# Performance work log

Hardware: AMD Instinct MI355X
Metric: run time of the kernel (lower is better)

## Reference

```python
import jax, jax.numpy as jnp
import numpy as np

DIM = 128
NUM_HEADS = 4
WIN = 16  # effective window: window_size(8) * sqrt(dim_t=4)
N = WIN * WIN
B_ = 512
NW = 64


def _relative_position_index(wh, ww):
    coords = np.stack(np.meshgrid(np.arange(wh), np.arange(ww), indexing='ij'))  # (2,wh,ww)
    cf = coords.reshape(2, -1)
    rel = cf[:, :, None] - cf[:, None, :]  # (2,N,N)
    rel = rel.transpose(1, 2, 0).copy()
    rel[:, :, 0] += wh - 1
    rel[:, :, 1] += ww - 1
    rel[:, :, 0] *= 2 * ww - 1
    return rel.sum(-1).astype(np.int32)  # (N,N)


def setup_inputs() -> dict:
    key = jax.random.key(0)
    ks = jax.random.split(key, 7)
    inputs = jax.random.normal(ks[0], (B_, N, DIM), dtype=jnp.float32)
    mask = jax.random.normal(ks[1], (NW, N, N), dtype=jnp.float32)
    qkv_w = jax.random.normal(ks[2], (3 * DIM, DIM), dtype=jnp.float32) * 0.02
    qkv_b = jnp.zeros((3 * DIM,), dtype=jnp.float32)
    proj_w = jax.random.normal(ks[3], (DIM, DIM), dtype=jnp.float32) * 0.02
    proj_b = jnp.zeros((DIM,), dtype=jnp.float32)
    table_sz = (2 * WIN - 1) * (2 * WIN - 1)  # 961
    bias_table = jax.random.normal(ks[4], (table_sz, NUM_HEADS), dtype=jnp.float32) * 0.02
    rel_idx = jnp.asarray(_relative_position_index(WIN, WIN))  # (N,N) int32
    return {"inputs": inputs, "mask": mask, "qkv_w": qkv_w, "qkv_b": qkv_b,
            "proj_w": proj_w, "proj_b": proj_b, "bias_table": bias_table,
            "rel_idx": rel_idx}


def reference(inputs, mask, qkv_w, qkv_b, proj_w, proj_b, bias_table, rel_idx):
    B, Nn, C = inputs.shape
    H = bias_table.shape[1]
    Dh = C // H
    scale = Dh ** -0.5
    qkv = (inputs @ qkv_w.T + qkv_b).reshape(B, Nn, 3, H, Dh)
    qkv = jnp.transpose(qkv, (2, 0, 3, 1, 4))  # (3,B,H,N,Dh)
    q, k, v = qkv[0] * scale, qkv[1], qkv[2]
    attn = jnp.einsum('bhnd,bhmd->bhnm', q, k)  # (B,H,N,N)
    rpb = jnp.transpose(bias_table[rel_idx], (2, 0, 1))  # (H,N,N)
    attn = attn + rpb[None]
    nW = mask.shape[0]
    attn = attn.reshape(B // nW, nW, H, Nn, Nn) + mask[None, :, None]
    attn = jax.nn.softmax(attn.reshape(B, H, Nn, Nn), axis=-1)
    out = jnp.einsum('bhnm,bhmd->bhnd', attn, v)
    out = jnp.transpose(out, (0, 2, 1, 3)).reshape(B, Nn, C)
    return out @ proj_w.T + proj_b
```

## Files before the change

kernel.cpp:

```cpp
#include <hip/hip_runtime.h>

typedef __bf16 bf16;
typedef __bf16 bf16x8 __attribute__((ext_vector_type(8)));
typedef __bf16 bf16x4 __attribute__((ext_vector_type(4)));
typedef float f32x4 __attribute__((ext_vector_type(4)));

static __device__ __forceinline__ f32x4 mfma16(bf16x8 a, bf16x8 b, f32x4 c) {
  return __builtin_amdgcn_mfma_f32_16x16x32_bf16(a, b, c, 0, 0, 0);
}

static __device__ __forceinline__ bf16x8 ld_bf8(const float* __restrict__ p) {
  f32x4 a = *(const f32x4*)p;
  f32x4 b = *(const f32x4*)(p + 4);
  bf16x8 r;
  r[0] = (bf16)a[0]; r[1] = (bf16)a[1]; r[2] = (bf16)a[2]; r[3] = (bf16)a[3];
  r[4] = (bf16)b[0]; r[5] = (bf16)b[1]; r[6] = (bf16)b[2]; r[7] = (bf16)b[3];
  return r;
}

__global__ void k0w(const float* __restrict__ qw, const float* __restrict__ pw,
                    bf16* __restrict__ wb, bf16* __restrict__ pwb) {
  int t = blockIdx.x * 256 + threadIdx.x;
  if (t < 12288) {
    f32x4 v = *(const f32x4*)(qw + (size_t)t * 4);
    bf16x4 o;
#pragma unroll
    for (int r = 0; r < 4; ++r) o[r] = (bf16)v[r];
    *(bf16x4*)(wb + (size_t)t * 4) = o;
  } else {
    int u = t - 12288;
    f32x4 v = *(const f32x4*)(pw + (size_t)u * 4);
    bf16x4 o;
#pragma unroll
    for (int r = 0; r < 4; ++r) o[r] = (bf16)v[r];
    *(bf16x4*)(pwb + (size_t)u * 4) = o;
  }
}

__global__ void __launch_bounds__(256, 4)
k1f(const float* __restrict__ x, const bf16* __restrict__ wb,
    const float* __restrict__ qb, bf16* __restrict__ q_s, bf16* __restrict__ k_s,
    bf16* __restrict__ vt, const float* __restrict__ mask,
    const float* __restrict__ bt, const int* __restrict__ ri,
    bf16* __restrict__ mb, bf16* __restrict__ rb) {
  const int bid = blockIdx.x;
  const int tid = threadIdx.x;
  if (bid >= 2048) {
    if (bid < 3072) {
      const int mid = bid - 2048;
#pragma unroll
      for (int it = 0; it < 4; ++it) {
        const size_t t = (size_t)mid * 1024 + it * 256 + tid;
        f32x4 m4 = *(const f32x4*)(mask + t * 4);
        bf16x4 o;
#pragma unroll
        for (int r = 0; r < 4; ++r) o[r] = (bf16)m4[r];
        *(bf16x4*)(mb + t * 4) = o;
      }
    } else {
      const int t = (bid - 3072) * 256 + tid;
      const int idx = ri[t];
      f32x4 v = *(const f32x4*)(bt + idx * 4);
#pragma unroll
      for (int h = 0; h < 4; ++h) rb[h * 65536 + t] = (bf16)v[h];
    }
    return;
  }

  const int b = bid & 511, qt = bid >> 9;
  const int wv = tid >> 6, ln = tid & 15, qd = (tid >> 4) & 3;
  const int row0 = qt * 64 + (wv >> 1) * 32;
  const int cg = wv & 1;

  bf16x8 xf[2][4];
#pragma unroll
  for (int nt = 0; nt < 2; ++nt)
#pragma unroll
    for (int ks = 0; ks < 4; ++ks)
      xf[nt][ks] = ld_bf8(x + (size_t)(b * 256 + row0 + nt * 16 + ln) * 128 +
                          ks * 32 + qd * 8);

#pragma unroll
  for (int ch = 0; ch < 2; ++ch) {
    f32x4 acc[4][2];
#pragma unroll
    for (int mt = 0; mt < 4; ++mt)
#pragma unroll
      for (int nt = 0; nt < 2; ++nt) acc[mt][nt] = (f32x4){0.f, 0.f, 0.f, 0.f};
#pragma unroll
    for (int mt = 0; mt < 4; ++mt)
#pragma unroll
      for (int ks = 0; ks < 4; ++ks) {
        bf16x8 wf = *(const bf16x8*)(wb + (size_t)(ch * 128 + cg * 64 + mt * 16 + ln) *
                                              128 + ks * 32 + qd * 8);
#pragma unroll
        for (int nt = 0; nt < 2; ++nt) acc[mt][nt] = mfma16(wf, xf[nt][ks], acc[mt][nt]);
      }
    bf16* dst = ch ? k_s : q_s;
    const float scl = ch ? 1.0f : 0.17677669529663689f;
#pragma unroll
    for (int mt = 0; mt < 4; ++mt) {
      const int c0 = cg * 64 + mt * 16 + qd * 4;
      f32x4 b4 = *(const f32x4*)(qb + ch * 128 + c0);
      const int hh = c0 >> 5, d0 = c0 & 31;
#pragma unroll
      for (int nt = 0; nt < 2; ++nt) {
        const int nr = row0 + nt * 16 + ln;
        bf16x4 o;
#pragma unroll
        for (int r = 0; r < 4; ++r) o[r] = (bf16)((acc[mt][nt][r] + b4[r]) * scl);
        *(bf16x4*)(dst + (size_t)((b * 4 + hh) * 256 + nr) * 32 + d0) = o;
      }
    }
  }

  f32x4 av[2][4];
#pragma unroll
  for (int nt = 0; nt < 2; ++nt)
#pragma unroll
    for (int mt = 0; mt < 4; ++mt) av[nt][mt] = (f32x4){0.f, 0.f, 0.f, 0.f};
#pragma unroll
  for (int ks = 0; ks < 4; ++ks)
#pragma unroll
    for (int mt = 0; mt < 4; ++mt) {
      bf16x8 wf = *(const bf16x8*)(wb + (size_t)(256 + cg * 64 + mt * 16 + ln) * 128 +
                                   ks * 32 + qd * 8);
#pragma unroll
      for (int nt = 0; nt < 2; ++nt) av[nt][mt] = mfma16(xf[nt][ks], wf, av[nt][mt]);
    }
#pragma unroll
  for (int nt = 0; nt < 2; ++nt)
#pragma unroll
    for (int mt = 0; mt < 4; ++mt) {
      const int c = cg * 64 + mt * 16 + ln;
      const float bb = qb[256 + c];
      const int hh = c >> 5, dd = c & 31;
      const int n0 = row0 + nt * 16 + qd * 4;
      bf16x4 o;
#pragma unroll
      for (int r = 0; r < 4; ++r) o[r] = (bf16)(av[nt][mt][r] + bb);
      *(bf16x4*)(vt + (size_t)((b * 4 + hh) * 32 + dd) * 256 + n0) = o;
    }
}

__global__ void __launch_bounds__(256, 2)
k2_attn(bf16* __restrict__ q_s, const bf16* __restrict__ k_s,
        const bf16* __restrict__ vt, const bf16* __restrict__ mb,
        const bf16* __restrict__ rb) {
  __shared__ bf16 ksm[256 * 32];
  __shared__ bf16 vsm[32 * 256];
  __shared__ bf16 psm[4 * 16 * 256];
  const int tid = threadIdx.x, wv = tid >> 6;
  const int ln = tid & 15, qd = (tid >> 4) & 3;
  const int w = blockIdx.x & 63, h = (blockIdx.x >> 6) & 3, rh = blockIdx.x >> 8;

  bf16x4 cmb[2][16];
#pragma unroll
  for (int si = 0; si < 2; ++si) {
    const int n = (rh * 8 + wv * 2 + si) * 16 + ln;
#pragma unroll
    for (int mt = 0; mt < 16; ++mt) {
      bf16x4 m4 = *(const bf16x4*)(mb + (size_t)(w * 256 + n) * 256 + mt * 16 + qd * 4);
      bf16x4 r4 = *(const bf16x4*)(rb + (size_t)h * 65536 + n * 256 + mt * 16 + qd * 4);
      bf16x4 cv;
#pragma unroll
      for (int r = 0; r < 4; ++r) cv[r] = (bf16)((float)m4[r] + (float)r4[r]);
      cmb[si][mt] = cv;
    }
  }

  for (int ib = 0; ib < 8; ++ib) {
    const int b = w + ib * 64;
    const bf16* kp = k_s + (size_t)(b * 4 + h) * 8192;
    const bf16* vp = vt + (size_t)(b * 4 + h) * 8192;
    __syncthreads();
#pragma unroll
    for (int i = 0; i < 4; ++i) {
      const int ci = i * 256 + tid;
      {
        const int r_ = ci >> 2, cb = ci & 3;
        *(bf16x8*)(ksm + r_ * 32 + ((cb ^ (r_ & 3)) * 8)) =
            *(const bf16x8*)(kp + r_ * 32 + cb * 8);
      }
      {
        const int r_ = ci >> 5, cb = ci & 31;
        *(bf16x8*)(vsm + r_ * 256 + ((cb ^ (r_ & 7)) * 8)) =
            *(const bf16x8*)(vp + r_ * 256 + cb * 8);
      }
    }
    __syncthreads();

#pragma unroll
    for (int si = 0; si < 2; ++si) {
      const int s = rh * 8 + wv * 2 + si;
      bf16x8 qf = *(const bf16x8*)(q_s + (size_t)(b * 4 + h) * 8192 +
                                   (s * 16 + ln) * 32 + qd * 8);
      f32x4 acc[16];
#pragma unroll
      for (int mt = 0; mt < 16; ++mt) acc[mt] = (f32x4){0.f, 0.f, 0.f, 0.f};
#pragma unroll
      for (int mt = 0; mt < 16; ++mt) {
        const int m = mt * 16 + ln;
        bf16x8 af = *(const bf16x8*)(ksm + m * 32 + ((qd ^ (m & 3)) * 8));
        acc[mt] = mfma16(af, qf, acc[mt]);
      }
      float sum = 0.f;
      bf16* pb = psm + wv * 4096 + ln * 256;
#pragma unroll
      for (int mt = 0; mt < 16; ++mt) {
        bf16x4 pv;
#pragma unroll
        for (int r = 0; r < 4; ++r) {
          float p = __expf(acc[mt][r] + (float)cmb[si][mt][r]);
          sum += p;
          pv[r] = (bf16)p;
        }
        *(bf16x4*)(pb + (((mt * 2 + (qd >> 1)) ^ (ln & 7)) * 8) + (qd & 1) * 4) = pv;
      }
      sum += __shfl_xor(sum, 16);
      sum += __shfl_xor(sum, 32);
      const float linv = 1.0f / sum;

      f32x4 accO[2];
      accO[0] = (f32x4){0.f, 0.f, 0.f, 0.f};
      accO[1] = (f32x4){0.f, 0.f, 0.f, 0.f};
#pragma unroll
      for (int kt = 0; kt < 8; ++kt) {
        bf16x8 pf = *(const bf16x8*)(pb + (((kt * 4 + qd) ^ (ln & 7)) * 8));
#pragma unroll
        for (int ct = 0; ct < 2; ++ct) {
          const int d = ct * 16 + ln;
          bf16x8 vf = *(const bf16x8*)(vsm + d * 256 + (((kt * 4 + qd) ^ (d & 7)) * 8));
          accO[ct] = mfma16(pf, vf, accO[ct]);
        }
      }
#pragma unroll
      for (int r = 0; r < 4; ++r) {
        const float lb = __shfl(linv, qd * 4 + r);
        const size_t obase =
            (size_t)(b * 4 + h) * 8192 + (size_t)(s * 16 + qd * 4 + r) * 32;
#pragma unroll
        for (int ct = 0; ct < 2; ++ct)
          q_s[obase + ct * 16 + ln] = (bf16)(accO[ct][r] * lb);
      }
    }
  }
}

__global__ void __launch_bounds__(256, 4)
k3_proj(const bf16* __restrict__ xb, const bf16* __restrict__ pwb,
        const float* __restrict__ pbias, float* __restrict__ out) {
  const int bid = blockIdx.x;
  const int b = bid & 511, qt = bid >> 9;
  const int tid = threadIdx.x;
  const int wv = tid >> 6, ln = tid & 15, qd = (tid >> 4) & 3;
  const int cg = wv & 1;
  const int row0 = qt * 64 + (wv >> 1) * 32;

  bf16x8 xf[2][4];
#pragma unroll
  for (int nt = 0; nt < 2; ++nt) {
    const int n = row0 + nt * 16 + ln;
#pragma unroll
    for (int ks = 0; ks < 4; ++ks)
      xf[nt][ks] = *(const bf16x8*)(xb + ((size_t)(b * 4 + ks) * 256 + n) * 32 + qd * 8);
  }

  f32x4 acc[4][2];
#pragma unroll
  for (int mt = 0; mt < 4; ++mt)
#pragma unroll
    for (int nt = 0; nt < 2; ++nt) acc[mt][nt] = (f32x4){0.f, 0.f, 0.f, 0.f};
#pragma unroll
  for (int mt = 0; mt < 4; ++mt)
#pragma unroll
    for (int ks = 0; ks < 4; ++ks) {
      bf16x8 wf = *(const bf16x8*)(pwb + (size_t)(cg * 64 + mt * 16 + ln) * 128 +
                                   ks * 32 + qd * 8);
#pragma unroll
      for (int nt = 0; nt < 2; ++nt) acc[mt][nt] = mfma16(wf, xf[nt][ks], acc[mt][nt]);
    }
#pragma unroll
  for (int mt = 0; mt < 4; ++mt) {
    const int c0 = cg * 64 + mt * 16 + qd * 4;
    f32x4 b4 = *(const f32x4*)(pbias + c0);
#pragma unroll
    for (int nt = 0; nt < 2; ++nt) {
      f32x4 o;
#pragma unroll
      for (int r = 0; r < 4; ++r) o[r] = acc[mt][nt][r] + b4[r];
      *(f32x4*)(out + (size_t)(b * 256 + row0 + nt * 16 + ln) * 128 + c0) = o;
    }
  }
}

extern "C" void kernel_launch(void* const* d_in, const int* in_sizes, int n_in,
                              void* d_out, int out_size, void* d_ws, size_t ws_size,
                              hipStream_t stream) {
  const float* x = (const float*)d_in[0];
  const float* mask = (const float*)d_in[1];
  const float* qkv_w = (const float*)d_in[2];
  const float* qkv_b = (const float*)d_in[3];
  const float* proj_w = (const float*)d_in[4];
  const float* proj_b = (const float*)d_in[5];
  const float* bias_table = (const float*)d_in[6];
  const int* rel_idx = (const int*)d_in[7];

  char* ws = (char*)d_ws;
  bf16* q_s = (bf16*)ws;
  bf16* k_s = (bf16*)(ws + 33554432);
  bf16* vt = (bf16*)(ws + 2ll * 33554432);
  bf16* wb = (bf16*)(ws + 3ll * 33554432);
  bf16* pwb = (bf16*)(ws + 3ll * 33554432 + 98304);
  bf16* mb = (bf16*)d_out;
  bf16* rb = (bf16*)((char*)d_out + 16777216);

  k0w<<<dim3(64), dim3(256), 0, stream>>>(qkv_w, proj_w, wb, pwb);
  k1f<<<dim3(3328), dim3(256), 0, stream>>>(x, wb, qkv_b, q_s, k_s, vt, mask,
                                            bias_table, rel_idx, mb, rb);
  k2_attn<<<dim3(512), dim3(256), 0, stream>>>(q_s, k_s, vt, mb, rb);
  k3_proj<<<dim3(2048), dim3(256), 0, stream>>>(q_s, pwb, proj_b, (float*)d_out);
}
```

Before: 303.6 us.

## Fuse QKV projection, window attention and output projection into one kernel

Replaces the separate QKV, attention and projection kernels with one kernel per batch window of 512 threads. Each block computes Q/K/V per head straight into shared memory, runs attention, and accumulates the output projection in registers before writing the final fp32 output. This removes the global round-trips of Q, K, V and the attention output. It also drops the bf16 mask pre-conversion and reads the fp32 mask directly each time. The cost is heavier per-block work, more register pressure, and repeated mask reads across heads.

```diff
diff --git a/kernel.cpp b/kernel.cpp
--- a/kernel.cpp
+++ b/kernel.cpp
@@ -18,280 +18,233 @@
   return r;
 }
 
-__global__ void k0w(const float* __restrict__ qw, const float* __restrict__ pw,
-                    bf16* __restrict__ wb, bf16* __restrict__ pwb) {
-  int t = blockIdx.x * 256 + threadIdx.x;
-  if (t < 12288) {
-    f32x4 v = *(const f32x4*)(qw + (size_t)t * 4);
-    bf16x4 o;
-#pragma unroll
-    for (int r = 0; r < 4; ++r) o[r] = (bf16)v[r];
-    *(bf16x4*)(wb + (size_t)t * 4) = o;
+__global__ void k0_prep(const float* __restrict__ qw, const float* __restrict__ pw,
+                        const float* __restrict__ bt, const int* __restrict__ ri,
+                        bf16* __restrict__ wb, bf16* __restrict__ pwb,
+                        bf16* __restrict__ rb) {
+  const int t = blockIdx.x * 256 + threadIdx.x;
+  if (blockIdx.x < 64) {
+    if (t < 12288) {
+      f32x4 v = *(const f32x4*)(qw + (size_t)t * 4);
+      bf16x4 o;
+#pragma unroll
+      for (int r = 0; r < 4; ++r) o[r] = (bf16)v[r];
+      *(bf16x4*)(wb + (size_t)t * 4) = o;
+    } else {
+      const int u = t - 12288;
+      f32x4 v = *(const f32x4*)(pw + (size_t)u * 4);
+      bf16x4 o;
+#pragma unroll
+      for (int r = 0; r < 4; ++r) o[r] = (bf16)v[r];
+      *(bf16x4*)(pwb + (size_t)u * 4) = o;
+    }
   } else {
-    int u = t - 12288;
-    f32x4 v = *(const f32x4*)(pw + (size_t)u * 4);
-    bf16x4 o;
-#pragma unroll
-    for (int r = 0; r < 4; ++r) o[r] = (bf16)v[r];
-    *(bf16x4*)(pwb + (size_t)u * 4) = o;
+    const int t2 = t - 16384;
+    const int idx = ri[t2];
+    f32x4 v = *(const f32x4*)(bt + idx * 4);
+#pragma unroll
+    for (int h = 0; h < 4; ++h) rb[h * 65536 + t2] = (bf16)v[h];
   }
 }
 
-__global__ void __launch_bounds__(256, 4)
-k1f(const float* __restrict__ x, const bf16* __restrict__ wb,
-    const float* __restrict__ qb, bf16* __restrict__ q_s, bf16* __restrict__ k_s,
-    bf16* __restrict__ vt, const float* __restrict__ mask,
-    const float* __restrict__ bt, const int* __restrict__ ri,
-    bf16* __restrict__ mb, bf16* __restrict__ rb) {
-  const int bid = blockIdx.x;
-  const int tid = threadIdx.x;
-  if (bid >= 2048) {
-    if (bid < 3072) {
-      const int mid = bid - 2048;
-#pragma unroll
-      for (int it = 0; it < 4; ++it) {
-        const size_t t = (size_t)mid * 1024 + it * 256 + tid;
-        f32x4 m4 = *(const f32x4*)(mask + t * 4);
-        bf16x4 o;
-#pragma unroll
-        for (int r = 0; r < 4; ++r) o[r] = (bf16)m4[r];
-        *(bf16x4*)(mb + t * 4) = o;
-      }
-    } else {
-      const int t = (bid - 3072) * 256 + tid;
-      const int idx = ri[t];
-      f32x4 v = *(const f32x4*)(bt + idx * 4);
-#pragma unroll
-      for (int h = 0; h < 4; ++h) rb[h * 65536 + t] = (bf16)v[h];
-    }
-    return;
-  }
-
-  const int b = bid & 511, qt = bid >> 9;
-  const int wv = tid >> 6, ln = tid & 15, qd = (tid >> 4) & 3;
-  const int row0 = qt * 64 + (wv >> 1) * 32;
-  const int cg = wv & 1;
-
-  bf16x8 xf[2][4];
-#pragma unroll
-  for (int nt = 0; nt < 2; ++nt)
-#pragma unroll
-    for (int ks = 0; ks < 4; ++ks)
-      xf[nt][ks] = ld_bf8(x + (size_t)(b * 256 + row0 + nt * 16 + ln) * 128 +
-                          ks * 32 + qd * 8);
-
-#pragma unroll
-  for (int ch = 0; ch < 2; ++ch) {
-    f32x4 acc[4][2];
-#pragma unroll
-    for (int mt = 0; mt < 4; ++mt)
-#pragma unroll
-      for (int nt = 0; nt < 2; ++nt) acc[mt][nt] = (f32x4){0.f, 0.f, 0.f, 0.f};
-#pragma unroll
-    for (int mt = 0; mt < 4; ++mt)
-#pragma unroll
-      for (int ks = 0; ks < 4; ++ks) {
-        bf16x8 wf = *(const bf16x8*)(wb + (size_t)(ch * 128 + cg * 64 + mt * 16 + ln) *
-                                              128 + ks * 32 + qd * 8);
-#pragma unroll
-        for (int nt = 0; nt < 2; ++nt) acc[mt][nt] = mfma16(wf, xf[nt][ks], acc[mt][nt]);
-      }
-    bf16* dst = ch ? k_s : q_s;
-    const float scl = ch ? 1.0f : 0.17677669529663689f;
-#pragma unroll
-    for (int mt = 0; mt < 4; ++mt) {
-      const int c0 = cg * 64 + mt * 16 + qd * 4;
-      f32x4 b4 = *(const f32x4*)(qb + ch * 128 + c0);
-      const int hh = c0 >> 5, d0 = c0 & 31;
-#pragma unroll
-      for (int nt = 0; nt < 2; ++nt) {
-        const int nr = row0 + nt * 16 + ln;
-        bf16x4 o;
-#pragma unroll
-        for (int r = 0; r < 4; ++r) o[r] = (bf16)((acc[mt][nt][r] + b4[r]) * scl);
-        *(bf16x4*)(dst + (size_t)((b * 4 + hh) * 256 + nr) * 32 + d0) = o;
-      }
-    }
-  }
-
-  f32x4 av[2][4];
-#pragma unroll
-  for (int nt = 0; nt < 2; ++nt)
-#pragma unroll
-    for (int mt = 0; mt < 4; ++mt) av[nt][mt] = (f32x4){0.f, 0.f, 0.f, 0.f};
-#pragma unroll
-  for (int ks = 0; ks < 4; ++ks)
-#pragma unroll
-    for (int mt = 0; mt < 4; ++mt) {
-      bf16x8 wf = *(const bf16x8*)(wb + (size_t)(256 + cg * 64 + mt * 16 + ln) * 128 +
-                                   ks * 32 + qd * 8);
-#pragma unroll
-      for (int nt = 0; nt < 2; ++nt) av[nt][mt] = mfma16(xf[nt][ks], wf, av[nt][mt]);
-    }
-#pragma unroll
-  for (int nt = 0; nt < 2; ++nt)
-#pragma unroll
-    for (int mt = 0; mt < 4; ++mt) {
-      const int c = cg * 64 + mt * 16 + ln;
-      const float bb = qb[256 + c];
-      const int hh = c >> 5, dd = c & 31;
-      const int n0 = row0 + nt * 16 + qd * 4;
-      bf16x4 o;
-#pragma unroll
-      for (int r = 0; r < 4; ++r) o[r] = (bf16)(av[nt][mt][r] + bb);
-      *(bf16x4*)(vt + (size_t)((b * 4 + hh) * 32 + dd) * 256 + n0) = o;
-    }
-}
-
-__global__ void __launch_bounds__(256, 2)
-k2_attn(bf16* __restrict__ q_s, const bf16* __restrict__ k_s,
-        const bf16* __restrict__ vt, const bf16* __restrict__ mb,
-        const bf16* __restrict__ rb) {
+__global__ void __launch_bounds__(512, 2)
+k_main(const float* __restrict__ x, const bf16* __restrict__ wb,
+       const float* __restrict__ qb, const bf16* __restrict__ pwb,
+       const float* __restrict__ pbias, const float* __restrict__ mask,
+       const bf16* __restrict__ rb, float* __restrict__ out) {
   __shared__ bf16 ksm[256 * 32];
   __shared__ bf16 vsm[32 * 256];
-  __shared__ bf16 psm[4 * 16 * 256];
+  __shared__ bf16 psm[8 * 2048];
   const int tid = threadIdx.x, wv = tid >> 6;
   const int ln = tid & 15, qd = (tid >> 4) & 3;
-  const int w = blockIdx.x & 63, h = (blockIdx.x >> 6) & 3, rh = blockIdx.x >> 8;
-
-  bf16x4 cmb[2][16];
-#pragma unroll
-  for (int si = 0; si < 2; ++si) {
-    const int n = (rh * 8 + wv * 2 + si) * 16 + ln;
-#pragma unroll
-    for (int mt = 0; mt < 16; ++mt) {
-      bf16x4 m4 = *(const bf16x4*)(mb + (size_t)(w * 256 + n) * 256 + mt * 16 + qd * 4);
-      bf16x4 r4 = *(const bf16x4*)(rb + (size_t)h * 65536 + n * 256 + mt * 16 + qd * 4);
-      bf16x4 cv;
-#pragma unroll
-      for (int r = 0; r < 4; ++r) cv[r] = (bf16)((float)m4[r] + (float)r4[r]);
-      cmb[si][mt] = cv;
-    }
-  }
-
-  for (int ib = 0; ib < 8; ++ib) {
-    const int b = w + ib * 64;
-    const bf16* kp = k_s + (size_t)(b * 4 + h) * 8192;
-    const bf16* vp = vt + (size_t)(b * 4 + h) * 8192;
+  const int b = blockIdx.x, w = b & 63;
+  bf16* pw_ = psm + wv * 2048;
+
+  bf16x8 xf[2][4];
+#pragma unroll
+  for (int nt = 0; nt < 2; ++nt)
+#pragma unroll
+    for (int ks = 0; ks < 4; ++ks)
+      xf[nt][ks] = ld_bf8(x + (size_t)(b * 256 + wv * 32 + nt * 16 + ln) * 128 +
+                          ks * 32 + qd * 8);
+
+  f32x4 acc_out[2][8];
+#pragma unroll
+  for (int si = 0; si < 2; ++si)
+#pragma unroll
+    for (int ct2 = 0; ct2 < 8; ++ct2) acc_out[si][ct2] = (f32x4){0.f, 0.f, 0.f, 0.f};
+
+  for (int h = 0; h < 4; ++h) {
+    {
+      f32x4 aq[2][2];
+#pragma unroll
+      for (int ct = 0; ct < 2; ++ct)
+#pragma unroll
+        for (int nt = 0; nt < 2; ++nt) aq[ct][nt] = (f32x4){0.f, 0.f, 0.f, 0.f};
+#pragma unroll
+      for (int ct = 0; ct < 2; ++ct)
+#pragma unroll
+        for (int ks = 0; ks < 4; ++ks) {
+          bf16x8 wf = *(const bf16x8*)(wb + (size_t)(h * 32 + ct * 16 + ln) * 128 +
+                                       ks * 32 + qd * 8);
+#pragma unroll
+          for (int nt = 0; nt < 2; ++nt) aq[ct][nt] = mfma16(wf, xf[nt][ks], aq[ct][nt]);
+        }
+#pragma unroll
+      for (int ct = 0; ct < 2; ++ct) {
+        const int c0 = ct * 16 + qd * 4;
+        f32x4 b4 = *(const f32x4*)(qb + h * 32 + c0);
+#pragma unroll
+        for (int nt = 0; nt < 2; ++nt) {
+          bf16x4 o;
+#pragma unroll
+          for (int r = 0; r < 4; ++r)
+            o[r] = (bf16)((aq[ct][nt][r] + b4[r]) * 0.17677669529663689f);
+          *(bf16x4*)(pw_ + (nt * 16 + ln) * 32 + c0) = o;
+        }
+      }
+    }
+    bf16x8 qf0 = *(const bf16x8*)(pw_ + (0 * 16 + ln) * 32 + qd * 8);
+    bf16x8 qf1 = *(const bf16x8*)(pw_ + (1 * 16 + ln) * 32 + qd * 8);
+
     __syncthreads();
-#pragma unroll
-    for (int i = 0; i < 4; ++i) {
-      const int ci = i * 256 + tid;
-      {
-        const int r_ = ci >> 2, cb = ci & 3;
-        *(bf16x8*)(ksm + r_ * 32 + ((cb ^ (r_ & 3)) * 8)) =
-            *(const bf16x8*)(kp + r_ * 32 + cb * 8);
-      }
-      {
-        const int r_ = ci >> 5, cb = ci & 31;
-        *(bf16x8*)(vsm + r_ * 256 + ((cb ^ (r_ & 7)) * 8)) =
-            *(const bf16x8*)(vp + r_ * 256 + cb * 8);
-      }
+
+    {
+      f32x4 ak[2][2];
+#pragma unroll
+      for (int ct = 0; ct < 2; ++ct)
+#pragma unroll
+        for (int nt = 0; nt < 2; ++nt) ak[ct][nt] = (f32x4){0.f, 0.f, 0.f, 0.f};
+#pragma unroll
+      for (int ct = 0; ct < 2; ++ct)
+#pragma unroll
+        for (int ks = 0; ks < 4; ++ks) {
+          bf16x8 wf = *(const bf16x8*)(wb + (size_t)(128 + h * 32 + ct * 16 + ln) * 128 +
+                                       ks * 32 + qd * 8);
+#pragma unroll
+          for (int nt = 0; nt < 2; ++nt) ak[ct][nt] = mfma16(wf, xf[nt][ks], ak[ct][nt]);
+        }
+#pragma unroll
+      for (int ct = 0; ct < 2; ++ct) {
+        const int c0 = ct * 16 + qd * 4;
+        f32x4 b4 = *(const f32x4*)(qb + 128 + h * 32 + c0);
+        const int slot = ct * 2 + (qd >> 1), off = (qd & 1) * 4;
+#pragma unroll
+        for (int nt = 0; nt < 2; ++nt) {
+          const int grow = wv * 32 + nt * 16 + ln;
+          bf16x4 o;
+#pragma unroll
+          for (int r = 0; r < 4; ++r) o[r] = (bf16)(ak[ct][nt][r] + b4[r]);
+          *(bf16x4*)(ksm + grow * 32 + ((slot ^ (grow & 3)) * 8) + off) = o;
+        }
+      }
+      f32x4 av[2][2];
+#pragma unroll
+      for (int nt = 0; nt < 2; ++nt)
+#pragma unroll
+        for (int ct = 0; ct < 2; ++ct) av[nt][ct] = (f32x4){0.f, 0.f, 0.f, 0.f};
+#pragma unroll
+      for (int ks = 0; ks < 4; ++ks)
+#pragma unroll
+        for (int ct = 0; ct < 2; ++ct) {
+          bf16x8 wf = *(const bf16x8*)(wb + (size_t)(256 + h * 32 + ct * 16 + ln) * 128 +
+                                       ks * 32 + qd * 8);
+#pragma unroll
+          for (int nt = 0; nt < 2; ++nt) av[nt][ct] = mfma16(xf[nt][ks], wf, av[nt][ct]);
+        }
+#pragma unroll
+      for (int nt = 0; nt < 2; ++nt)
+#pragma unroll
+        for (int ct = 0; ct < 2; ++ct) {
+          const int c = ct * 16 + ln;
+          const float bb = qb[256 + h * 32 + c];
+          const int n0 = wv * 32 + nt * 16 + qd * 4;
+          const int slot = n0 >> 3, off = (qd & 1) * 4;
+          bf16x4 o;
+#pragma unroll
+          for (int r = 0; r < 4; ++r) o[r] = (bf16)(av[nt][ct][r] + bb);
+          *(bf16x4*)(vsm + c * 256 + ((slot ^ (c & 7)) * 8) + off) = o;
+        }
     }
     __syncthreads();
 
 #pragma unroll
     for (int si = 0; si < 2; ++si) {
-      const int s = rh * 8 + wv * 2 + si;
-      bf16x8 qf = *(const bf16x8*)(q_s + (size_t)(b * 4 + h) * 8192 +
-                                   (s * 16 + ln) * 32 + qd * 8);
-      f32x4 acc[16];
-#pragma unroll
-      for (int mt = 0; mt < 16; ++mt) acc[mt] = (f32x4){0.f, 0.f, 0.f, 0.f};
-#pragma unroll
-      for (int mt = 0; mt < 16; ++mt) {
-        const int m = mt * 16 + ln;
-        bf16x8 af = *(const bf16x8*)(ksm + m * 32 + ((qd ^ (m & 3)) * 8));
-        acc[mt] = mfma16(af, qf, acc[mt]);
-      }
+      const bf16x8 qf = si ? qf1 : qf0;
+      const int n = wv * 32 + si * 16 + ln;
       float sum = 0.f;
-      bf16* pb = psm + wv * 4096 + ln * 256;
-#pragma unroll
-      for (int mt = 0; mt < 16; ++mt) {
-        bf16x4 pv;
-#pragma unroll
-        for (int r = 0; r < 4; ++r) {
-          float p = __expf(acc[mt][r] + (float)cmb[si][mt][r]);
-          sum += p;
-          pv[r] = (bf16)p;
-        }
-        *(bf16x4*)(pb + (((mt * 2 + (qd >> 1)) ^ (ln & 7)) * 8) + (qd & 1) * 4) = pv;
+      f32x4 accO[2];
+      accO[0] = (f32x4){0.f, 0.f, 0.f, 0.f};
+      accO[1] = (f32x4){0.f, 0.f, 0.f, 0.f};
+#pragma unroll
+      for (int hf = 0; hf < 2; ++hf) {
+        f32x4 acc[8];
+#pragma unroll
+        for (int mt = 0; mt < 8; ++mt) acc[mt] = (f32x4){0.f, 0.f, 0.f, 0.f};
+#pragma unroll
+        for (int mt = 0; mt < 8; ++mt) {
+          const int m = hf * 128 + mt * 16 + ln;
+          bf16x8 af = *(const bf16x8*)(ksm + m * 32 + ((qd ^ (m & 3)) * 8));
+          acc[mt] = mfma16(af, qf, acc[mt]);
+        }
+#pragma unroll
+        for (int mt = 0; mt < 8; ++mt) {
+          const int mcol = hf * 128 + mt * 16 + qd * 4;
+          f32x4 m4 = *(const f32x4*)(mask + ((size_t)w * 256 + n) * 256 + mcol);
+          bf16x4 r4 = *(const bf16x4*)(rb + (size_t)h * 65536 + n * 256 + mcol);
+          bf16x4 pv;
+#pragma unroll
+          for (int r = 0; r < 4; ++r) {
+            float p = __expf(acc[mt][r] + m4[r] + (float)r4[r]);
+            sum += p;
+            pv[r] = (bf16)p;
+          }
+          *(bf16x4*)(pw_ + ln * 128 + (((mt * 2 + (qd >> 1)) ^ (ln & 7)) * 8) +
+                     (qd & 1) * 4) = pv;
+        }
+#pragma unroll
+        for (int ktl = 0; ktl < 4; ++ktl) {
+          const int kt = hf * 4 + ktl;
+          bf16x8 pf = *(const bf16x8*)(pw_ + ln * 128 + (((ktl * 4 + qd) ^ (ln & 7)) * 8));
+#pragma unroll
+          for (int ct = 0; ct < 2; ++ct) {
+            const int d = ct * 16 + ln;
+            bf16x8 vf = *(const bf16x8*)(vsm + d * 256 + (((kt * 4 + qd) ^ (d & 7)) * 8));
+            accO[ct] = mfma16(pf, vf, accO[ct]);
+          }
+        }
       }
       sum += __shfl_xor(sum, 16);
       sum += __shfl_xor(sum, 32);
       const float linv = 1.0f / sum;
-
-      f32x4 accO[2];
-      accO[0] = (f32x4){0.f, 0.f, 0.f, 0.f};
-      accO[1] = (f32x4){0.f, 0.f, 0.f, 0.f};
-#pragma unroll
-      for (int kt = 0; kt < 8; ++kt) {
-        bf16x8 pf = *(const bf16x8*)(pb + (((kt * 4 + qd) ^ (ln & 7)) * 8));
-#pragma unroll
-        for (int ct = 0; ct < 2; ++ct) {
-          const int d = ct * 16 + ln;
-          bf16x8 vf = *(const bf16x8*)(vsm + d * 256 + (((kt * 4 + qd) ^ (d & 7)) * 8));
-          accO[ct] = mfma16(pf, vf, accO[ct]);
-        }
-      }
 #pragma unroll
       for (int r = 0; r < 4; ++r) {
         const float lb = __shfl(linv, qd * 4 + r);
-        const size_t obase =
-            (size_t)(b * 4 + h) * 8192 + (size_t)(s * 16 + qd * 4 + r) * 32;
 #pragma unroll
         for (int ct = 0; ct < 2; ++ct)
-          q_s[obase + ct * 16 + ln] = (bf16)(accO[ct][r] * lb);
+          pw_[(qd * 4 + r) * 40 + ct * 16 + ln] = (bf16)(accO[ct][r] * lb);
+      }
+      bf16x8 aof = *(const bf16x8*)(pw_ + ln * 40 + qd * 8);
+#pragma unroll
+      for (int ct2 = 0; ct2 < 8; ++ct2) {
+        bf16x8 wpf = *(const bf16x8*)(pwb + (size_t)(ct2 * 16 + ln) * 128 + h * 32 +
+                                      qd * 8);
+        acc_out[si][ct2] = mfma16(aof, wpf, acc_out[si][ct2]);
       }
     }
   }
-}
-
-__global__ void __launch_bounds__(256, 4)
-k3_proj(const bf16* __restrict__ xb, const bf16* __restrict__ pwb,
-        const float* __restrict__ pbias, float* __restrict__ out) {
-  const int bid = blockIdx.x;
-  const int b = bid & 511, qt = bid >> 9;
-  const int tid = threadIdx.x;
-  const int wv = tid >> 6, ln = tid & 15, qd = (tid >> 4) & 3;
-  const int cg = wv & 1;
-  const int row0 = qt * 64 + (wv >> 1) * 32;
-
-  bf16x8 xf[2][4];
-#pragma unroll
-  for (int nt = 0; nt < 2; ++nt) {
-    const int n = row0 + nt * 16 + ln;
-#pragma unroll
-    for (int ks = 0; ks < 4; ++ks)
-      xf[nt][ks] = *(const bf16x8*)(xb + ((size_t)(b * 4 + ks) * 256 + n) * 32 + qd * 8);
-  }
-
-  f32x4 acc[4][2];
-#pragma unroll
-  for (int mt = 0; mt < 4; ++mt)
-#pragma unroll
-    for (int nt = 0; nt < 2; ++nt) acc[mt][nt] = (f32x4){0.f, 0.f, 0.f, 0.f};
-#pragma unroll
-  for (int mt = 0; mt < 4; ++mt)
-#pragma unroll
-    for (int ks = 0; ks < 4; ++ks) {
-      bf16x8 wf = *(const bf16x8*)(pwb + (size_t)(cg * 64 + mt * 16 + ln) * 128 +
-                                   ks * 32 + qd * 8);
-#pragma unroll
-      for (int nt = 0; nt < 2; ++nt) acc[mt][nt] = mfma16(wf, xf[nt][ks], acc[mt][nt]);
-    }
-#pragma unroll
-  for (int mt = 0; mt < 4; ++mt) {
-    const int c0 = cg * 64 + mt * 16 + qd * 4;
-    f32x4 b4 = *(const f32x4*)(pbias + c0);
-#pragma unroll
-    for (int nt = 0; nt < 2; ++nt) {
-      f32x4 o;
-#pragma unroll
-      for (int r = 0; r < 4; ++r) o[r] = acc[mt][nt][r] + b4[r];
-      *(f32x4*)(out + (size_t)(b * 256 + row0 + nt * 16 + ln) * 128 + c0) = o;
-    }
-  }
+
+#pragma unroll
+  for (int si = 0; si < 2; ++si)
+#pragma unroll
+    for (int ct2 = 0; ct2 < 8; ++ct2) {
+      const int col = ct2 * 16 + ln;
+      const float bb = pbias[col];
+#pragma unroll
+      for (int r = 0; r < 4; ++r)
+        out[(size_t)(b * 256 + wv * 32 + si * 16 + qd * 4 + r) * 128 + col] =
+            acc_out[si][ct2][r] + bb;
+    }
 }
 
 extern "C" void kernel_launch(void* const* d_in, const int* in_sizes, int n_in,
@@ -307,17 +260,12 @@
   const int* rel_idx = (const int*)d_in[7];
 
   char* ws = (char*)d_ws;
-  bf16* q_s = (bf16*)ws;
-  bf16* k_s = (bf16*)(ws + 33554432);
-  bf16* vt = (bf16*)(ws + 2ll * 33554432);
-  bf16* wb = (bf16*)(ws + 3ll * 33554432);
-  bf16* pwb = (bf16*)(ws + 3ll * 33554432 + 98304);
-  bf16* mb = (bf16*)d_out;
-  bf16* rb = (bf16*)((char*)d_out + 16777216);
-
-  k0w<<<dim3(64), dim3(256), 0, stream>>>(qkv_w, proj_w, wb, pwb);
-  k1f<<<dim3(3328), dim3(256), 0, stream>>>(x, wb, qkv_b, q_s, k_s, vt, mask,
-                                            bias_table, rel_idx, mb, rb);
-  k2_attn<<<dim3(512), dim3(256), 0, stream>>>(q_s, k_s, vt, mb, rb);
-  k3_proj<<<dim3(2048), dim3(256), 0, stream>>>(q_s, pwb, proj_b, (float*)d_out);
-}
+  bf16* wb = (bf16*)ws;
+  bf16* pwb = (bf16*)(ws + 98304);
+  bf16* rb = (bf16*)(ws + 131072);
+
+  k0_prep<<<dim3(320), dim3(256), 0, stream>>>(qkv_w, proj_w, bias_table, rel_idx,
+                                               wb, pwb, rb);
+  k_main<<<dim3(512), dim3(512), 0, stream>>>(x, wb, qkv_b, pwb, proj_b, mask, rb,
+                                              (float*)d_out);
+}
```

Measured after the change: 374.2 us. 1.23x slower.
